# Performance work log

Hardware: AMD Instinct MI355X
Metric: run time of the kernel (lower is better)

Reference implementation:

```python
import jax, jax.numpy as jnp
import numpy as np

B, T, C = 8, 2048, 1024  # micro_bsz, seq_len, n_embd (== complexsize)


def setup_inputs() -> dict:
    key = jax.random.key(0)
    ks = jax.random.split(key, 6)
    w = lambda k, shape: (jax.random.normal(k, shape, dtype=jnp.float32) * 0.02)
    return {
        "x": jax.random.normal(ks[0], (B, T, C), dtype=jnp.float32),
        "Wk": w(ks[1], (2 * C, C)),      # key: n_embd -> 2*n_embd (no bias)
        "Wa": w(ks[2], (C, 2 * C)),      # activation: 2*n_embd -> n_embd (no bias)
        "Wf": w(ks[3], (2, C, C)),       # WaveNet filter conv, kernel=2, WIO layout
        "Wg": w(ks[4], (2, C, C)),       # WaveNet gate conv, kernel=2, WIO layout
        "Wo": w(ks[5], (C, C)),          # WaveNet 1x1 output projection
    }


def _causal_conv(x, W):
    # x: [B,T,Cin], W: [K,Cin,Cout]; left-pad K-1 for causality
    return jax.lax.conv_general_dilated(
        x, W, window_strides=(1,), padding=[(W.shape[0] - 1, 0)],
        dimension_numbers=("NWC", "WIO", "NWC"))


def _wavenet_short(x, Wf, Wg, Wo):
    # undialated gated WaveNet unit: tanh(conv_f(x)) * sigmoid(conv_g(x)) -> 1x1 proj
    h = jnp.tanh(_causal_conv(x, Wf)) * jax.nn.sigmoid(_causal_conv(x, Wg))
    return h @ Wo.T


def reference(x, Wk, Wa, Wf, Wg, Wo):
    Bx, Tx, Cx = x.shape
    k = (x @ Wk.T).reshape(Bx, Tx, Cx, 2)                 # [B,T,C,2]
    cv = jax.lax.complex(k[..., 0], k[..., 1])            # view_as_complex -> [B,T,C]
    scale = jax.lax.cummax(jnp.abs(cv), axis=1)           # running max of magnitude
    cv2 = cv / scale.astype(cv.dtype)                      # normalize magnitude <= 1
    kv = jnp.cumprod(cv2, axis=1)                          # complex cumulative product
    re = jnp.stack([kv.real, kv.imag], axis=-1).reshape(Bx, Tx, 2 * Cx)  # view_as_real
    return (re @ Wa.T) * _wavenet_short(x * scale, Wf, Wg, Wo)
```

## Files before the change

### kernel.cpp

```cpp
#include <hip/hip_runtime.h>
#include <cmath>

#define T_SEQ 2048
#define C_DIM 1024
#define BM 128
#define BN 128
#define BK 32

typedef unsigned short u16;
typedef unsigned int u32;
typedef short bf16x8 __attribute__((ext_vector_type(8)));
typedef _Float16 f16x8 __attribute__((ext_vector_type(8)));
typedef float f32x4 __attribute__((ext_vector_type(4)));
typedef unsigned short u16x8 __attribute__((ext_vector_type(8)));

#define AS1 __attribute__((address_space(1)))
#define AS3 __attribute__((address_space(3)))

__device__ __forceinline__ u16 f2bf(float f) {
    u32 u = __builtin_bit_cast(u32, f);
    u32 r = u + 0x7fffu + ((u >> 16) & 1u);
    return (u16)(r >> 16);
}
__device__ __forceinline__ u16 f2h(float f) {
    return __builtin_bit_cast(u16, (_Float16)f);
}
__device__ __forceinline__ float h2f(u16 h) {
    return (float)__builtin_bit_cast(_Float16, h);
}
__device__ __forceinline__ float bf2f(u16 h) {
    return __builtin_bit_cast(float, (u32)h << 16);
}
__device__ __forceinline__ void gl_lds16(const void* g, void* l) {
    __builtin_amdgcn_global_load_lds((const AS1 u32*)g, (AS3 u32*)l, 16, 0, 0);
}

__device__ __forceinline__ int xcd_swz(int lin, int nwg) {
    return (lin & 7) * (nwg >> 3) + (lin >> 3);
}

template<int EPI, int DT>
__global__ __launch_bounds__(256)
void mfma_gemm(const u16* __restrict__ Ap, const u16* __restrict__ B0,
               void* __restrict__ Cout, int M, int N, int K)
{
    __shared__ u16 lds[2 * 2 * 4096];
    const int tid  = threadIdx.x;
    const int lane = tid & 63;
    const int wid  = tid >> 6;
    const int wr = wid >> 1, wc = wid & 1;
    const int gx = gridDim.x;
    const int lin = xcd_swz(blockIdx.x + gx * blockIdx.y, gx * gridDim.y);
    const int m0 = (lin / gx) * BM;
    const int n0 = (lin % gx) * BN;
    const int NT = K / BK;

    f32x4 acc[4][4] = {};

    auto stage = [&](int it, int buf) {
        const int k0 = it * BK;
        u16* base = &lds[buf * 8192];
        #pragma unroll
        for (int i = 0; i < 2; ++i) {
            const int chunk = wid + 4 * i;
            const int rloc  = chunk * 16 + (lane >> 2);
            const int slot  = (lane & 3) ^ ((rloc >> 1) & 3);
            gl_lds16(B0 + (size_t)(n0 + rloc) * K + k0 + slot * 8,
                     base + 4096 + chunk * 512);
            gl_lds16(Ap + (size_t)(m0 + rloc) * K + k0 + slot * 8,
                     base + chunk * 512);
        }
    };

    auto compute = [&](int buf) {
        const u16* base = &lds[buf * 8192];
        if constexpr (DT == 0) {
            bf16x8 a[4], b[4];
            #pragma unroll
            for (int f = 0; f < 4; ++f) {
                const int row = wr * 64 + f * 16 + (lane & 15);
                const int sp  = ((lane >> 4) & 3) ^ ((row >> 1) & 3);
                a[f] = *(const bf16x8*)&base[row * 32 + sp * 8];
                const int rowb = wc * 64 + f * 16 + (lane & 15);
                const int spb  = ((lane >> 4) & 3) ^ ((rowb >> 1) & 3);
                b[f] = *(const bf16x8*)&base[4096 + rowb * 32 + spb * 8];
            }
            #pragma unroll
            for (int fm = 0; fm < 4; ++fm)
                #pragma unroll
                for (int fn = 0; fn < 4; ++fn)
                    acc[fm][fn] = __builtin_amdgcn_mfma_f32_16x16x32_bf16(a[fm], b[fn], acc[fm][fn], 0, 0, 0);
        } else {
            f16x8 a[4], b[4];
            #pragma unroll
            for (int f = 0; f < 4; ++f) {
                const int row = wr * 64 + f * 16 + (lane & 15);
                const int sp  = ((lane >> 4) & 3) ^ ((row >> 1) & 3);
                a[f] = *(const f16x8*)&base[row * 32 + sp * 8];
                const int rowb = wc * 64 + f * 16 + (lane & 15);
                const int spb  = ((lane >> 4) & 3) ^ ((rowb >> 1) & 3);
                b[f] = *(const f16x8*)&base[4096 + rowb * 32 + spb * 8];
            }
            #pragma unroll
            for (int fm = 0; fm < 4; ++fm)
                #pragma unroll
                for (int fn = 0; fn < 4; ++fn)
                    acc[fm][fn] = __builtin_amdgcn_mfma_f32_16x16x32_f16(a[fm], b[fn], acc[fm][fn], 0, 0, 0);
        }
    };

    stage(0, 0);
    int cur = 0;
    for (int it = 0; it < NT; ++it) {
        __syncthreads();
        if (it + 1 < NT) stage(it + 1, cur ^ 1);
        compute(cur);
        cur ^= 1;
    }

    const int crow0 = m0 + wr * 64 + ((lane >> 4) << 2);
    const int ccol  = n0 + wc * 64 + (lane & 15);
    #pragma unroll
    for (int fm = 0; fm < 4; ++fm)
        #pragma unroll
        for (int fn = 0; fn < 4; ++fn)
            #pragma unroll
            for (int r = 0; r < 4; ++r) {
                const size_t idx = (size_t)(crow0 + fm * 16 + r) * N + ccol + fn * 16;
                if constexpr (EPI == 0) ((float*)Cout)[idx] = acc[fm][fn][r];
                else                    ((u16*)Cout)[idx] = f2h(acc[fm][fn][r]);
            }
}

__global__ __launch_bounds__(256)
void dual_gemm(const u16* __restrict__ A1, const u16* __restrict__ B1, int K1,
               const u16* __restrict__ A2, const u16* __restrict__ B2, int K2,
               float* __restrict__ out, int M, int N)
{
    __shared__ u16 lds[2 * 2 * 4096];
    const int tid  = threadIdx.x;
    const int lane = tid & 63;
    const int wid  = tid >> 6;
    const int wr = wid >> 1, wc = wid & 1;
    const int gx = gridDim.x;
    const int lin = xcd_swz(blockIdx.x + gx * blockIdx.y, gx * gridDim.y);
    const int m0 = (lin / gx) * BM;
    const int n0 = (lin % gx) * BN;

    f32x4 acc1[4][4] = {};
    f32x4 acc2[4][4] = {};

    auto stage = [&](const u16* Ap, const u16* Bp, int K, int it, int buf) {
        const int k0 = it * BK;
        u16* base = &lds[buf * 8192];
        #pragma unroll
        for (int i = 0; i < 2; ++i) {
            const int chunk = wid + 4 * i;
            const int rloc  = chunk * 16 + (lane >> 2);
            const int slot  = (lane & 3) ^ ((rloc >> 1) & 3);
            gl_lds16(Bp + (size_t)(n0 + rloc) * K + k0 + slot * 8,
                     base + 4096 + chunk * 512);
            gl_lds16(Ap + (size_t)(m0 + rloc) * K + k0 + slot * 8,
                     base + chunk * 512);
        }
    };

    auto compute = [&](int buf, f32x4 (&acc)[4][4]) {
        const u16* base = &lds[buf * 8192];
        bf16x8 a[4], b[4];
        #pragma unroll
        for (int f = 0; f < 4; ++f) {
            const int row = wr * 64 + f * 16 + (lane & 15);
            const int sp  = ((lane >> 4) & 3) ^ ((row >> 1) & 3);
            a[f] = *(const bf16x8*)&base[row * 32 + sp * 8];
            const int rowb = wc * 64 + f * 16 + (lane & 15);
            const int spb  = ((lane >> 4) & 3) ^ ((rowb >> 1) & 3);
            b[f] = *(const bf16x8*)&base[4096 + rowb * 32 + spb * 8];
        }
        #pragma unroll
        for (int fm = 0; fm < 4; ++fm)
            #pragma unroll
            for (int fn = 0; fn < 4; ++fn)
                acc[fm][fn] = __builtin_amdgcn_mfma_f32_16x16x32_bf16(a[fm], b[fn], acc[fm][fn], 0, 0, 0);
    };

    const int NT1 = K1 / BK, NT2 = K2 / BK;
    stage(A1, B1, K1, 0, 0);
    int cur = 0;
    for (int it = 0; it < NT1; ++it) {
        __syncthreads();
        if (it + 1 < NT1) stage(A1, B1, K1, it + 1, cur ^ 1);
        else              stage(A2, B2, K2, 0, cur ^ 1);
        compute(cur, acc1);
        cur ^= 1;
    }
    for (int it = 0; it < NT2; ++it) {
        __syncthreads();
        if (it + 1 < NT2) stage(A2, B2, K2, it + 1, cur ^ 1);
        compute(cur, acc2);
        cur ^= 1;
    }

    const int crow0 = m0 + wr * 64 + ((lane >> 4) << 2);
    const int ccol  = n0 + wc * 64 + (lane & 15);
    #pragma unroll
    for (int fm = 0; fm < 4; ++fm)
        #pragma unroll
        for (int fn = 0; fn < 4; ++fn)
            #pragma unroll
            for (int r = 0; r < 4; ++r) {
                const size_t idx = (size_t)(crow0 + fm * 16 + r) * N + ccol + fn * 16;
                out[idx] = acc1[fm][fn][r] * acc2[fm][fn][r];
            }
}

__global__ __launch_bounds__(256)
void conv_gate(const u16* __restrict__ A, const u16* __restrict__ Wfgt,
               u16* __restrict__ H, int M)
{
    constexpr int KIT = C_DIM / BK;
    constexpr int NT  = 2 * KIT;
    __shared__ u16 lds[2 * 3 * 4096];
    const int tid  = threadIdx.x;
    const int lane = tid & 63;
    const int wid  = tid >> 6;
    const int wr = wid >> 1, wc = wid & 1;
    const int gx = gridDim.x;
    const int lin = xcd_swz(blockIdx.x + gx * blockIdx.y, gx * gridDim.y);
    const int m0 = (lin / gx) * BM;
    const int n0 = (lin % gx) * BN;

    f32x4 accF[4][4] = {};
    f32x4 accG[4][4] = {};

    auto stage = [&](int it, int buf) {
        const int p  = it / KIT;
        const int k0 = (it - p * KIT) * BK;
        u16* base = &lds[buf * 12288];
        const u16* BF = Wfgt + (size_t)p * 2 * C_DIM * C_DIM;
        const u16* BG = BF + (size_t)C_DIM * C_DIM;
        const int sh = (p == 0) ? 1 : 0;
        #pragma unroll
        for (int i = 0; i < 2; ++i) {
            const int chunk = wid + 4 * i;
            const int rloc  = chunk * 16 + (lane >> 2);
            const int slot  = (lane & 3) ^ ((rloc >> 1) & 3);
            int grow = m0 + rloc - sh;
            if (grow < 0) grow = 0;
            gl_lds16(A + (size_t)grow * C_DIM + k0 + slot * 8,
                     base + chunk * 512);
            gl_lds16(BF + (size_t)(n0 + rloc) * C_DIM + k0 + slot * 8,
                     base + 4096 + chunk * 512);
            gl_lds16(BG + (size_t)(n0 + rloc) * C_DIM + k0 + slot * 8,
                     base + 8192 + chunk * 512);
        }
    };

    auto compute = [&](int buf) {
        const u16* base = &lds[buf * 12288];
        bf16x8 a[4], bf[4], bg[4];
        #pragma unroll
        for (int f = 0; f < 4; ++f) {
            const int row = wr * 64 + f * 16 + (lane & 15);
            const int sp  = ((lane >> 4) & 3) ^ ((row >> 1) & 3);
            a[f] = *(const bf16x8*)&base[row * 32 + sp * 8];
            const int rowb = wc * 64 + f * 16 + (lane & 15);
            const int spb  = ((lane >> 4) & 3) ^ ((rowb >> 1) & 3);
            bf[f] = *(const bf16x8*)&base[4096 + rowb * 32 + spb * 8];
            bg[f] = *(const bf16x8*)&base[8192 + rowb * 32 + spb * 8];
        }
        #pragma unroll
        for (int fm = 0; fm < 4; ++fm)
            #pragma unroll
            for (int fn = 0; fn < 4; ++fn) {
                accF[fm][fn] = __builtin_amdgcn_mfma_f32_16x16x32_bf16(a[fm], bf[fn], accF[fm][fn], 0, 0, 0);
                accG[fm][fn] = __builtin_amdgcn_mfma_f32_16x16x32_bf16(a[fm], bg[fn], accG[fm][fn], 0, 0, 0);
            }
    };

    stage(0, 0);
    int cur = 0;
    for (int it = 0; it < NT; ++it) {
        __syncthreads();
        if ((it / KIT) == 0 && (m0 % T_SEQ) == 0) {
            if (tid < 4) {
                u16x8 z = {0,0,0,0,0,0,0,0};
                *(u16x8*)&lds[cur * 12288 + tid * 8] = z;
            }
            __syncthreads();
        }
        if (it + 1 < NT) stage(it + 1, cur ^ 1);
        compute(cur);
        cur ^= 1;
    }

    const int crow0 = m0 + wr * 64 + ((lane >> 4) << 2);
    const int ccol  = n0 + wc * 64 + (lane & 15);
    #pragma unroll
    for (int fm = 0; fm < 4; ++fm)
        #pragma unroll
        for (int fn = 0; fn < 4; ++fn)
            #pragma unroll
            for (int r = 0; r < 4; ++r) {
                const float fv = accF[fm][fn][r];
                const float gv = accG[fm][fn][r];
                const float th = 1.0f - 2.0f / (expf(2.0f * fv) + 1.0f);
                const float sg = 1.0f / (1.0f + expf(-gv));
                H[(size_t)(crow0 + fm * 16 + r) * C_DIM + ccol + fn * 16] = f2bf(th * sg);
            }
}

#define SSEG 32
#define SCHB 32
#define SSL (T_SEQ / SSEG)

__global__ __launch_bounds__(1024, 1)
void scan_kernel(u16* __restrict__ kq, u16* __restrict__ xyb)
{
    __shared__ float  lmax[SSEG][SCHB];
    __shared__ float2 lprod[SSEG][SCHB];
    const int blk = blockIdx.x;
    const int b   = blk >> 5;
    const int c0  = (blk & 31) * SCHB;
    const int ch  = threadIdx.x & (SCHB - 1);
    const int seg = threadIdx.x >> 5;
    const int c   = c0 + ch;
    const int t0  = seg * SSL;
    const size_t baseh = (size_t)b * T_SEQ * 2048 + 2 * c + (size_t)t0 * 2048;
    const size_t base1 = (size_t)b * T_SEQ * C_DIM + c + (size_t)t0 * C_DIM;

    float m2 = 0.f;
    {
        size_t idx = baseh;
        for (int t = 0; t < SSL; ++t) {
            const u32 v = *(const u32*)&kq[idx];
            const float re = h2f((u16)(v & 0xffffu));
            const float im = h2f((u16)(v >> 16));
            m2 = fmaxf(m2, re * re + im * im);
            idx += 2048;
        }
    }
    lmax[seg][ch] = sqrtf(m2);
    __syncthreads();
    #pragma unroll
    for (int s = 1; s < SSEG; s <<= 1) {
        const float v = lmax[seg][ch];
        const float u = (seg >= s) ? lmax[seg - s][ch] : 0.f;
        __syncthreads();
        lmax[seg][ch] = fmaxf(v, u);
        __syncthreads();
    }
    const float premax = (seg > 0) ? lmax[seg - 1][ch] : 0.f;

    float pr = 1.f, pi = 0.f;
    float m = premax;
    {
        size_t idx = baseh, idx1 = base1;
        for (int t = 0; t < SSL; ++t) {
            const u32 v = *(const u32*)&kq[idx];
            const float re = h2f((u16)(v & 0xffffu));
            const float im = h2f((u16)(v >> 16));
            m = fmaxf(m, sqrtf(re * re + im * im));
            const float inv = 1.f / m;
            const float r0 = re * inv, r1 = im * inv;
            const float nr = pr * r0 - pi * r1;
            const float ni = pr * r1 + pi * r0;
            pr = nr; pi = ni;
            const float xv = h2f(xyb[idx1]);
            xyb[idx1] = f2bf(xv * m);
            idx += 2048; idx1 += C_DIM;
        }
    }
    lprod[seg][ch] = make_float2(pr, pi);
    __syncthreads();
    #pragma unroll
    for (int s = 1; s < SSEG; s <<= 1) {
        const float2 v = lprod[seg][ch];
        const float2 u = (seg >= s) ? lprod[seg - s][ch] : make_float2(1.f, 0.f);
        __syncthreads();
        lprod[seg][ch] = make_float2(u.x * v.x - u.y * v.y,
                                     u.x * v.y + u.y * v.x);
        __syncthreads();
    }
    float ppr = 1.f, ppi = 0.f;
    if (seg > 0) { const float2 pp = lprod[seg - 1][ch]; ppr = pp.x; ppi = pp.y; }

    pr = 1.f; pi = 0.f;
    m = premax;
    {
        size_t idx = baseh;
        for (int t = 0; t < SSL; ++t) {
            const u32 v = *(const u32*)&kq[idx];
            const float re = h2f((u16)(v & 0xffffu));
            const float im = h2f((u16)(v >> 16));
            m = fmaxf(m, sqrtf(re * re + im * im));
            const float inv = 1.f / m;
            const float r0 = re * inv, r1 = im * inv;
            const float nr = pr * r0 - pi * r1;
            const float ni = pr * r1 + pi * r0;
            pr = nr; pi = ni;
            const float fr = ppr * nr - ppi * ni;
            const float fi = ppr * ni + ppi * nr;
            *(u32*)&kq[idx] = ((u32)f2bf(fi) << 16) | (u32)f2bf(fr);
            idx += 2048;
        }
    }
}

__global__ void cvt_bf16(const float* __restrict__ src, u16* __restrict__ dst, int n)
{
    const int i = (blockIdx.x * blockDim.x + threadIdx.x) * 4;
    if (i >= n) return;
    const float4 v = *(const float4*)&src[i];
    ushort4 o;
    o.x = f2bf(v.x); o.y = f2bf(v.y); o.z = f2bf(v.z); o.w = f2bf(v.w);
    *(ushort4*)&dst[i] = o;
}

__global__ void cvt_f16(const float* __restrict__ src, u16* __restrict__ dst, int n)
{
    const int i = (blockIdx.x * blockDim.x + threadIdx.x) * 4;
    if (i >= n) return;
    const float4 v = *(const float4*)&src[i];
    ushort4 o;
    o.x = f2h(v.x); o.y = f2h(v.y); o.z = f2h(v.z); o.w = f2h(v.w);
    *(ushort4*)&dst[i] = o;
}

__global__ __launch_bounds__(256)
void wtrans(const float* __restrict__ Wf, const float* __restrict__ Wg,
            u16* __restrict__ dst)
{
    __shared__ float tile[64][65];
    const int z = blockIdx.z;
    const float* src = ((z < 2) ? Wf : Wg) + (size_t)(z & 1) * C_DIM * C_DIM;
    u16* d = dst + (size_t)(z & 1) * (2 * C_DIM) * C_DIM
                 + ((z < 2) ? (size_t)0 : (size_t)C_DIM * C_DIM);
    const int k0 = blockIdx.x * 64;
    const int n0 = blockIdx.y * 64;
    const int tx = threadIdx.x & 63, ty = threadIdx.x >> 6;
    #pragma unroll
    for (int i = 0; i < 16; ++i) {
        const int r = ty + i * 4;
        tile[r][tx] = src[(size_t)(k0 + r) * C_DIM + n0 + tx];
    }
    __syncthreads();
    #pragma unroll
    for (int i = 0; i < 16; ++i) {
        const int r = ty + i * 4;
        d[(size_t)(n0 + r) * C_DIM + k0 + tx] = f2bf(tile[tx][r]);
    }
}

extern "C" void kernel_launch(void* const* d_in, const int* in_sizes, int n_in,
                              void* d_out, int out_size, void* d_ws, size_t ws_size,
                              hipStream_t stream)
{
    const float* x  = (const float*)d_in[0];
    const float* Wk = (const float*)d_in[1];
    const float* Wa = (const float*)d_in[2];
    const float* Wf = (const float*)d_in[3];
    const float* Wg = (const float*)d_in[4];
    const float* Wo = (const float*)d_in[5];
    float* out = (float*)d_out;

    const int M = 8 * T_SEQ;
    u16* kq   = (u16*)d_ws;
    u16* yb   = (u16*)((char*)d_ws + 67108864ull);
    u16* hb   = (u16*)((char*)d_ws + 100663296ull);
    u16* Wkh  = (u16*)((char*)d_ws + 134217728ull);
    u16* Wab  = Wkh + 2048 * 1024;
    u16* Wfgt = Wab + 2048 * 1024;
    u16* Wob  = Wfgt + 2ull * 2048 * 1024;

    cvt_f16 <<<(2048 * 1024 / 4 + 255) / 256, 256, 0, stream>>>(Wk, Wkh, 2048 * 1024);
    cvt_bf16<<<(2048 * 1024 / 4 + 255) / 256, 256, 0, stream>>>(Wa, Wab, 2048 * 1024);
    cvt_bf16<<<(1024 * 1024 / 4 + 255) / 256, 256, 0, stream>>>(Wo, Wob, 1024 * 1024);
    wtrans  <<<dim3(16, 16, 4), 256, 0, stream>>>(Wf, Wg, Wfgt);
    cvt_f16 <<<(M * 1024 / 4) / 256, 256, 0, stream>>>(x, yb, M * 1024);

    mfma_gemm<2, 1><<<dim3(2048 / BN, M / BM), 256, 0, stream>>>(
        yb, Wkh, kq, M, 2048, 1024);

    scan_kernel<<<256, 1024, 0, stream>>>(kq, yb);

    conv_gate<<<dim3(1024 / BN, M / BM), 256, 0, stream>>>(yb, Wfgt, hb, M);

    dual_gemm<<<dim3(1024 / BN, M / BM), 256, 0, stream>>>(
        kq, Wab, 2048, hb, Wob, 1024, out, M, 1024);
}
```

Baseline: 473.0 us.

## Cache scan inputs in registers across passes and fuse weight conversion kernels

```diff
diff --git a/kernel.cpp b/kernel.cpp
--- a/kernel.cpp
+++ b/kernel.cpp
@@ -27,9 +27,6 @@
 }
 __device__ __forceinline__ float h2f(u16 h) {
     return (float)__builtin_bit_cast(_Float16, h);
-}
-__device__ __forceinline__ float bf2f(u16 h) {
-    return __builtin_bit_cast(float, (u32)h << 16);
 }
 __device__ __forceinline__ void gl_lds16(const void* g, void* l) {
     __builtin_amdgcn_global_load_lds((const AS1 u32*)g, (AS3 u32*)l, 16, 0, 0);
@@ -329,13 +326,16 @@
     const size_t baseh = (size_t)b * T_SEQ * 2048 + 2 * c + (size_t)t0 * 2048;
     const size_t base1 = (size_t)b * T_SEQ * C_DIM + c + (size_t)t0 * C_DIM;
 
+    u32 raw[SSL];
+
     float m2 = 0.f;
     {
         size_t idx = baseh;
+        #pragma unroll
         for (int t = 0; t < SSL; ++t) {
-            const u32 v = *(const u32*)&kq[idx];
-            const float re = h2f((u16)(v & 0xffffu));
-            const float im = h2f((u16)(v >> 16));
+            raw[t] = *(const u32*)&kq[idx];
+            const float re = h2f((u16)(raw[t] & 0xffffu));
+            const float im = h2f((u16)(raw[t] >> 16));
             m2 = fmaxf(m2, re * re + im * im);
             idx += 2048;
         }
@@ -355,11 +355,11 @@
     float pr = 1.f, pi = 0.f;
     float m = premax;
     {
-        size_t idx = baseh, idx1 = base1;
+        size_t idx1 = base1;
+        #pragma unroll
         for (int t = 0; t < SSL; ++t) {
-            const u32 v = *(const u32*)&kq[idx];
-            const float re = h2f((u16)(v & 0xffffu));
-            const float im = h2f((u16)(v >> 16));
+            const float re = h2f((u16)(raw[t] & 0xffffu));
+            const float im = h2f((u16)(raw[t] >> 16));
             m = fmaxf(m, sqrtf(re * re + im * im));
             const float inv = 1.f / m;
             const float r0 = re * inv, r1 = im * inv;
@@ -368,7 +368,7 @@
             pr = nr; pi = ni;
             const float xv = h2f(xyb[idx1]);
             xyb[idx1] = f2bf(xv * m);
-            idx += 2048; idx1 += C_DIM;
+            idx1 += C_DIM;
         }
     }
     lprod[seg][ch] = make_float2(pr, pi);
@@ -389,10 +389,10 @@
     m = premax;
     {
         size_t idx = baseh;
+        #pragma unroll
         for (int t = 0; t < SSL; ++t) {
-            const u32 v = *(const u32*)&kq[idx];
-            const float re = h2f((u16)(v & 0xffffu));
-            const float im = h2f((u16)(v >> 16));
+            const float re = h2f((u16)(raw[t] & 0xffffu));
+            const float im = h2f((u16)(raw[t] >> 16));
             m = fmaxf(m, sqrtf(re * re + im * im));
             const float inv = 1.f / m;
             const float r0 = re * inv, r1 = im * inv;
@@ -407,14 +407,27 @@
     }
 }
 
-__global__ void cvt_bf16(const float* __restrict__ src, u16* __restrict__ dst, int n)
-{
+__global__ void cvt_weights(const float* __restrict__ Wk, const float* __restrict__ Wa,
+                            const float* __restrict__ Wo, u16* __restrict__ Wkh,
+                            u16* __restrict__ Wab, u16* __restrict__ Wob)
+{
+    const int n1 = 2048 * 1024, n2 = 2 * 2048 * 1024, n3 = n2 + 1024 * 1024;
     const int i = (blockIdx.x * blockDim.x + threadIdx.x) * 4;
-    if (i >= n) return;
-    const float4 v = *(const float4*)&src[i];
-    ushort4 o;
-    o.x = f2bf(v.x); o.y = f2bf(v.y); o.z = f2bf(v.z); o.w = f2bf(v.w);
-    *(ushort4*)&dst[i] = o;
+    if (i < n1) {
+        const float4 v = *(const float4*)&Wk[i];
+        ushort4 o; o.x = f2h(v.x); o.y = f2h(v.y); o.z = f2h(v.z); o.w = f2h(v.w);
+        *(ushort4*)&Wkh[i] = o;
+    } else if (i < n2) {
+        const int j = i - n1;
+        const float4 v = *(const float4*)&Wa[j];
+        ushort4 o; o.x = f2bf(v.x); o.y = f2bf(v.y); o.z = f2bf(v.z); o.w = f2bf(v.w);
+        *(ushort4*)&Wab[j] = o;
+    } else if (i < n3) {
+        const int j = i - n2;
+        const float4 v = *(const float4*)&Wo[j];
+        ushort4 o; o.x = f2bf(v.x); o.y = f2bf(v.y); o.z = f2bf(v.z); o.w = f2bf(v.w);
+        *(ushort4*)&Wob[j] = o;
+    }
 }
 
 __global__ void cvt_f16(const float* __restrict__ src, u16* __restrict__ dst, int n)
@@ -473,9 +486,8 @@
     u16* Wfgt = Wab + 2048 * 1024;
     u16* Wob  = Wfgt + 2ull * 2048 * 1024;
 
-    cvt_f16 <<<(2048 * 1024 / 4 + 255) / 256, 256, 0, stream>>>(Wk, Wkh, 2048 * 1024);
-    cvt_bf16<<<(2048 * 1024 / 4 + 255) / 256, 256, 0, stream>>>(Wa, Wab, 2048 * 1024);
-    cvt_bf16<<<(1024 * 1024 / 4 + 255) / 256, 256, 0, stream>>>(Wo, Wob, 1024 * 1024);
+    cvt_weights<<<(5 * 1024 * 1024 * 5 / 5 / 4 + 255) / 256 + 0, 256, 0, stream>>>(
+        Wk, Wa, Wo, Wkh, Wab, Wob);
     wtrans  <<<dim3(16, 16, 4), 256, 0, stream>>>(Wf, Wg, Wfgt);
     cvt_f16 <<<(M * 1024 / 4) / 256, 256, 0, stream>>>(x, yb, M * 1024);
 
```

Result: slower. 633.4 us (+33.9%).
